# Performance work log

Hardware: AMD Instinct MI355X
Metric: run time of the kernel (lower is better)

Reference implementation:

```python
import jax, jax.numpy as jnp
import numpy as np

HIDDEN = 1024
HEADS = 16
HEAD_DIM = HIDDEN // HEADS


def setup_inputs() -> dict:
    key = jax.random.key(0)
    k1, k2, k3, k4, k5 = jax.random.split(key, 5)
    scale = 1.0 / np.sqrt(HIDDEN)
    return {
        "query": jax.random.normal(k1, (8, 1024, HIDDEN), dtype=jnp.float32),
        "w_qkv": jax.random.normal(k2, (HIDDEN, 3 * HIDDEN), dtype=jnp.float32) * scale,
        "b_qkv": jnp.zeros((3 * HIDDEN,), dtype=jnp.float32),
        "w_o": jax.random.normal(k3, (HIDDEN, HIDDEN), dtype=jnp.float32) * scale,
        "b_o": jnp.zeros((HIDDEN,), dtype=jnp.float32),
    }


def reference(query, w_qkv, b_qkv, w_o, b_o):
    B, S, _ = query.shape
    qkv = query @ w_qkv + b_qkv                      # [B,S,3H]
    q, k, v = jnp.split(qkv, 3, axis=-1)
    # split heads -> [B, heads, S, head_dim]
    def sh(x):
        return x.reshape(B, S, HEADS, HEAD_DIM).transpose(0, 2, 1, 3)
    qh, kh, vh = sh(q), sh(k), sh(v)
    qh = qh * (HEAD_DIM ** -0.5)
    logits = jnp.einsum("bhqd,bhkd->bhqk", qh, kh)   # [B,H,S,S]
    weights = jax.nn.softmax(logits, axis=-1)        # dropout p=0.0 -> identity
    x = jnp.einsum("bhqk,bhkd->bhqd", weights, vh)
    x = x.transpose(0, 2, 1, 3).reshape(B, S, HIDDEN)
    return x @ w_o + b_o
```

## Files before the change

kernel.cpp:

```cpp
#include <hip/hip_runtime.h>
#include <math.h>

#define BATCH   8
#define SEQ     1024
#define HIDDEN  1024
#define NHEADS  16
#define HDIM    64
#define MROWS   (BATCH * SEQ)

typedef __bf16 bf16x8 __attribute__((ext_vector_type(8)));
typedef float  f32x4  __attribute__((ext_vector_type(4)));

__device__ __forceinline__ unsigned short f2bf(float f) {
    union { float f; unsigned int u; } v; v.f = f;
    unsigned int u = v.u;
    u += 0x7fffu + ((u >> 16) & 1u);
    return (unsigned short)(u >> 16);
}

__device__ __forceinline__ unsigned int pack2bf_trunc(float a, float b) {
    union { float f; unsigned int u; } ua, ub;
    ua.f = a; ub.f = b;
    return (ua.u >> 16) | (ub.u & 0xFFFF0000u);
}

__device__ __forceinline__ void gl2lds16(const unsigned short* g, unsigned short* l) {
    __builtin_amdgcn_global_load_lds(
        (const __attribute__((address_space(1))) void*)g,
        (__attribute__((address_space(3))) void*)l, 16, 0, 0);
}

__global__ void cvt_f32_bf16_kernel(const float* __restrict__ in,
                                    unsigned short* __restrict__ out, int n4) {
    int i = blockIdx.x * blockDim.x + threadIdx.x;
    if (i < n4) {
        float4 v = reinterpret_cast<const float4*>(in)[i];
        ushort4 o;
        o.x = f2bf(v.x); o.y = f2bf(v.y); o.z = f2bf(v.z); o.w = f2bf(v.w);
        reinterpret_cast<ushort4*>(out)[i] = o;
    }
}

__global__ void transpose_cvt_kernel(const float* __restrict__ in,
                                     unsigned short* __restrict__ out,
                                     int R, int C) {
    __shared__ float tile[32][33];
    int x  = blockIdx.x * 32 + threadIdx.x;
    int y0 = blockIdx.y * 32;
#pragma unroll
    for (int j = 0; j < 32; j += 8)
        tile[threadIdx.y + j][threadIdx.x] = in[(size_t)(y0 + threadIdx.y + j) * C + x];
    __syncthreads();
    int x2 = y0 + threadIdx.x;
    int y2 = blockIdx.x * 32;
#pragma unroll
    for (int j = 0; j < 32; j += 8)
        out[(size_t)(y2 + threadIdx.y + j) * R + x2] = f2bf(tile[threadIdx.x][threadIdx.y + j]);
}

__global__ void transpose_v_kernel(const unsigned short* __restrict__ vin,
                                   unsigned short* __restrict__ vout) {
    __shared__ unsigned short tile[32][33];
    const int head = blockIdx.z;
    const int s0 = blockIdx.x * 32, d0 = blockIdx.y * 32;
    const unsigned short* src = vin + (size_t)head * SEQ * HDIM;
    unsigned short* dst = vout + (size_t)head * SEQ * HDIM;
    const int tx = threadIdx.x, ty = threadIdx.y;
#pragma unroll
    for (int j = 0; j < 32; j += 8)
        tile[ty + j][tx] = src[(size_t)(s0 + ty + j) * HDIM + d0 + tx];
    __syncthreads();
#pragma unroll
    for (int j = 0; j < 32; j += 8)
        dst[(size_t)(d0 + ty + j) * SEQ + s0 + tx] = tile[tx][ty + j];
}

template <int EPI>
__global__ __launch_bounds__(256) void gemm_bt_kernel(
    const unsigned short* __restrict__ A,
    const unsigned short* __restrict__ Bt,
    const float* __restrict__ bias,
    unsigned short* __restrict__ out_bf,
    float* __restrict__ out_f,
    int M, int N, int K) {
    __shared__ __align__(16) unsigned short As[128 * 64];
    __shared__ __align__(16) unsigned short Bs[128 * 64];

    const int tid  = threadIdx.x;
    const int wid  = tid >> 6;
    const int lane = tid & 63;
    const int l15  = lane & 15;
    const int quad = lane >> 4;
    const int wm   = (wid & 1) * 64;
    const int wn   = (wid >> 1) * 64;

    const int npn = N >> 7;
    const int pid = blockIdx.x;
    const int ppg = 4 * npn;
    const int gid = pid / ppg;
    const int loc = pid - gid * ppg;
    const int pm  = gid * 4 + (loc & 3);
    const int pn  = loc >> 2;
    const int m0  = pm * 128;
    const int n0  = pn * 128;

    const int srow = wid * 32 + (lane >> 3);
    const int skcs = ((lane & 7) ^ (lane >> 3)) * 8;
    const int rsw  = lane & 7;

    f32x4 acc[4][4];
#pragma unroll
    for (int i = 0; i < 4; ++i)
#pragma unroll
        for (int j = 0; j < 4; ++j) acc[i][j] = (f32x4){0.f, 0.f, 0.f, 0.f};

    for (int kt = 0; kt < K; kt += 64) {
        __syncthreads();
#pragma unroll
        for (int it = 0; it < 4; ++it) {
            int row = srow + it * 8;
            gl2lds16(A  + (size_t)(m0 + row) * K + kt + skcs, As + (wid * 32 + it * 8) * 64);
            gl2lds16(Bt + (size_t)(n0 + row) * K + kt + skcs, Bs + (wid * 32 + it * 8) * 64);
        }
        __syncthreads();
#pragma unroll
        for (int ks = 0; ks < 2; ++ks) {
            bf16x8 afr[4], bfr[4];
#pragma unroll
            for (int i = 0; i < 4; ++i)
                afr[i] = *reinterpret_cast<const bf16x8*>(
                    As + (wm + i * 16 + l15) * 64 + ((ks * 4 + quad) ^ rsw) * 8);
#pragma unroll
            for (int j = 0; j < 4; ++j)
                bfr[j] = *reinterpret_cast<const bf16x8*>(
                    Bs + (wn + j * 16 + l15) * 64 + ((ks * 4 + quad) ^ rsw) * 8);
#pragma unroll
            for (int i = 0; i < 4; ++i)
#pragma unroll
                for (int j = 0; j < 4; ++j)
                    acc[i][j] = __builtin_amdgcn_mfma_f32_16x16x32_bf16(afr[i], bfr[j], acc[i][j], 0, 0, 0);
        }
    }

#pragma unroll
    for (int j = 0; j < 4; ++j) {
        int col   = n0 + wn + j * 16 + l15;
        float bv  = bias[col];
        if constexpr (EPI == 0) {
            int which = col >> 10;
            int rem   = col & 1023;
            int h     = rem >> 6, d = rem & 63;
            float sc  = (which == 0) ? 0.18033688011112042f : 1.0f;
#pragma unroll
            for (int i = 0; i < 4; ++i)
#pragma unroll
                for (int r = 0; r < 4; ++r) {
                    int row = m0 + wm + i * 16 + quad * 4 + r;
                    int b   = row >> 10, s = row & 1023;
                    float v = (acc[i][j][r] + bv) * sc;
                    size_t idx = ((((size_t)which * BATCH + b) * NHEADS + h) * SEQ + s) * HDIM + d;
                    out_bf[idx] = f2bf(v);
                }
        } else {
#pragma unroll
            for (int i = 0; i < 4; ++i)
#pragma unroll
                for (int r = 0; r < 4; ++r) {
                    int row = m0 + wm + i * 16 + quad * 4 + r;
                    out_f[(size_t)row * N + col] = acc[i][j][r] + bv;
                }
        }
    }
}

__global__ __launch_bounds__(256, 4) void attn_kernel(
    const unsigned short* __restrict__ qkv,
    const unsigned short* __restrict__ vt,
    unsigned short* __restrict__ x) {
    constexpr int LDP = 68;
    __shared__ __align__(16) unsigned short Ks[64 * 64];
    __shared__ __align__(16) unsigned short Vs[64 * 64];
    __shared__ __align__(16) unsigned short PQ[4][32 * LDP];

    unsigned short* Qs = &PQ[0][0];

    const int tid  = threadIdx.x;
    const int wid  = tid >> 6;
    const int lane = tid & 63;
    const int l15  = lane & 15;
    const int quad = lane >> 4;
    const int srow8 = lane >> 3;
    const int skcs  = ((lane & 7) ^ srow8) * 8;
    const int rsw   = lane & 7;

    const int id = blockIdx.x;
    const int bh = (id & 7) * 16 + (id >> 6);
    const int q0 = ((id >> 3) & 7) * 128;

    const unsigned short* Qg  = qkv + (size_t)bh * SEQ * HDIM;
    const unsigned short* Kg  = qkv + (size_t)(128 + bh) * SEQ * HDIM;
    const unsigned short* VTg = vt + (size_t)bh * SEQ * HDIM;

#pragma unroll
    for (int it = 0; it < 4; ++it) {
        gl2lds16(Qg + (size_t)(q0 + wid * 32 + it * 8 + srow8) * HDIM + skcs,
                 Qs + (wid * 32 + it * 8) * 64);
    }
    __syncthreads();

    bf16x8 qf[2][2];
#pragma unroll
    for (int m = 0; m < 2; ++m)
#pragma unroll
        for (int h = 0; h < 2; ++h)
            qf[m][h] = *reinterpret_cast<const bf16x8*>(
                Qs + (wid * 32 + m * 16 + l15) * 64 + ((h * 4 + quad) ^ rsw) * 8);

    float lsum[2][4];
    f32x4 accO[2][4];
#pragma unroll
    for (int m = 0; m < 2; ++m)
#pragma unroll
        for (int r = 0; r < 4; ++r) lsum[m][r] = 0.f;
#pragma unroll
    for (int m = 0; m < 2; ++m)
#pragma unroll
        for (int jd = 0; jd < 4; ++jd) accO[m][jd] = (f32x4){0.f, 0.f, 0.f, 0.f};

    for (int t0 = 0; t0 < SEQ; t0 += 64) {
        __syncthreads();
#pragma unroll
        for (int it = 0; it < 2; ++it) {
            int row = wid * 16 + it * 8 + srow8;
            gl2lds16(Kg + (size_t)(t0 + row) * HDIM + skcs, Ks + (wid * 16 + it * 8) * 64);
            gl2lds16(VTg + (size_t)row * SEQ + t0 + skcs,   Vs + (wid * 16 + it * 8) * 64);
        }
        __syncthreads();

        f32x4 accL[2][4];
#pragma unroll
        for (int m = 0; m < 2; ++m)
#pragma unroll
            for (int j = 0; j < 4; ++j) accL[m][j] = (f32x4){0.f, 0.f, 0.f, 0.f};
#pragma unroll
        for (int j = 0; j < 4; ++j) {
            int krow = l15 * 4 + j;
            int kr7  = krow & 7;
            bf16x8 kf0 = *reinterpret_cast<const bf16x8*>(
                Ks + krow * 64 + ((0 + quad) ^ kr7) * 8);
            bf16x8 kf1 = *reinterpret_cast<const bf16x8*>(
                Ks + krow * 64 + ((4 + quad) ^ kr7) * 8);
#pragma unroll
            for (int m = 0; m < 2; ++m) {
                accL[m][j] = __builtin_amdgcn_mfma_f32_16x16x32_bf16(qf[m][0], kf0, accL[m][j], 0, 0, 0);
                accL[m][j] = __builtin_amdgcn_mfma_f32_16x16x32_bf16(qf[m][1], kf1, accL[m][j], 0, 0, 0);
            }
        }

#pragma unroll
        for (int m = 0; m < 2; ++m)
#pragma unroll
            for (int r = 0; r < 4; ++r) {
                float p0 = exp2f(accL[m][0][r]);
                float p1 = exp2f(accL[m][1][r]);
                float p2 = exp2f(accL[m][2][r]);
                float p3 = exp2f(accL[m][3][r]);
                lsum[m][r] += (p0 + p1) + (p2 + p3);
                uint2 pk;
                pk.x = pack2bf_trunc(p0, p1);
                pk.y = pack2bf_trunc(p2, p3);
                *reinterpret_cast<uint2*>(
                    &PQ[wid][(m * 16 + quad * 4 + r) * LDP + l15 * 4]) = pk;
            }

        bf16x8 pf[2][2];
#pragma unroll
        for (int m = 0; m < 2; ++m)
#pragma unroll
            for (int h = 0; h < 2; ++h)
                pf[m][h] = *reinterpret_cast<const bf16x8*>(
                    PQ[wid] + (m * 16 + l15) * LDP + h * 32 + quad * 8);
#pragma unroll
        for (int jd = 0; jd < 4; ++jd) {
            bf16x8 vf0 = *reinterpret_cast<const bf16x8*>(
                Vs + (jd * 16 + l15) * 64 + ((0 + quad) ^ rsw) * 8);
            bf16x8 vf1 = *reinterpret_cast<const bf16x8*>(
                Vs + (jd * 16 + l15) * 64 + ((4 + quad) ^ rsw) * 8);
#pragma unroll
            for (int m = 0; m < 2; ++m) {
                accO[m][jd] = __builtin_amdgcn_mfma_f32_16x16x32_bf16(pf[m][0], vf0, accO[m][jd], 0, 0, 0);
                accO[m][jd] = __builtin_amdgcn_mfma_f32_16x16x32_bf16(pf[m][1], vf1, accO[m][jd], 0, 0, 0);
            }
        }
    }

    const int b = bh >> 4, h = bh & 15;
#pragma unroll
    for (int m = 0; m < 2; ++m)
#pragma unroll
        for (int r = 0; r < 4; ++r) {
            float s = lsum[m][r];
            s += __shfl_xor(s, 1);
            s += __shfl_xor(s, 2);
            s += __shfl_xor(s, 4);
            s += __shfl_xor(s, 8);
            float inv = 1.0f / s;
            int srow = q0 + wid * 32 + m * 16 + quad * 4 + r;
            size_t base = ((size_t)b * SEQ + srow) * HIDDEN + h * HDIM;
#pragma unroll
            for (int jd = 0; jd < 4; ++jd)
                x[base + jd * 16 + l15] = f2bf(accO[m][jd][r] * inv);
        }
}

extern "C" void kernel_launch(void* const* d_in, const int* in_sizes, int n_in,
                              void* d_out, int out_size, void* d_ws, size_t ws_size,
                              hipStream_t stream) {
    const float* query = (const float*)d_in[0];
    const float* w_qkv = (const float*)d_in[1];
    const float* b_qkv = (const float*)d_in[2];
    const float* w_o   = (const float*)d_in[3];
    const float* b_o   = (const float*)d_in[4];
    float* out = (float*)d_out;

    unsigned short* ws = (unsigned short*)d_ws;
    unsigned short* queryBf = ws;
    unsigned short* wqkvT   = queryBf + (size_t)MROWS * HIDDEN;
    unsigned short* woT     = wqkvT + (size_t)3 * HIDDEN * HIDDEN;
    unsigned short* qkvbuf  = woT + (size_t)HIDDEN * HIDDEN;
    unsigned short* xbuf    = qkvbuf + (size_t)3 * MROWS * HIDDEN;
    unsigned short* vtbuf   = queryBf;

    cvt_f32_bf16_kernel<<<(MROWS * HIDDEN / 4 + 255) / 256, 256, 0, stream>>>(
        query, queryBf, MROWS * HIDDEN / 4);
    transpose_cvt_kernel<<<dim3(3 * HIDDEN / 32, HIDDEN / 32), dim3(32, 8), 0, stream>>>(
        w_qkv, wqkvT, HIDDEN, 3 * HIDDEN);
    transpose_cvt_kernel<<<dim3(HIDDEN / 32, HIDDEN / 32), dim3(32, 8), 0, stream>>>(
        w_o, woT, HIDDEN, HIDDEN);

    gemm_bt_kernel<0><<<dim3((MROWS / 128) * (3 * HIDDEN / 128)), 256, 0, stream>>>(
        queryBf, wqkvT, b_qkv, qkvbuf, nullptr, MROWS, 3 * HIDDEN, HIDDEN);

    transpose_v_kernel<<<dim3(SEQ / 32, HDIM / 32, BATCH * NHEADS), dim3(32, 8), 0, stream>>>(
        qkvbuf + (size_t)2 * BATCH * NHEADS * SEQ * HDIM, vtbuf);

    attn_kernel<<<dim3(1024), 256, 0, stream>>>(qkvbuf, vtbuf, xbuf);

    gemm_bt_kernel<1><<<dim3((MROWS / 128) * (HIDDEN / 128)), 256, 0, stream>>>(
        xbuf, woT, b_o, nullptr, out, MROWS, HIDDEN, HIDDEN);
}
```

Baseline: 255.4 us.

## Add 256x256-tile pipelined GEMM kernel for QKV projection

Adds a new GEMM kernel with 256x256 output tiles, 512 threads, a quad-buffered LDS staging scheme with direct global-to-LDS loads, XOR swizzle, and interleaved MFMA phases with priority hints. It also maps blocks to XCDs so each XCD works on a contiguous band of M tiles. It is used only for the QKV projection and is meant to raise data reuse and overlap loads with MFMA work. The trade-off is heavier register and LDS use, which limits occupancy, and the grid has fewer blocks (384).

```diff
diff --git a/kernel.cpp b/kernel.cpp
--- a/kernel.cpp
+++ b/kernel.cpp
@@ -169,6 +169,196 @@
                     int row = m0 + wm + i * 16 + quad * 4 + r;
                     out_f[(size_t)row * N + col] = acc[i][j][r] + bv;
                 }
+        }
+    }
+}
+
+template <int EPI>
+__global__ __launch_bounds__(512, 2) void gemm256_kernel(
+    const unsigned short* __restrict__ A,
+    const unsigned short* __restrict__ Bt,
+    const float* __restrict__ bias,
+    unsigned short* __restrict__ out_bf,
+    float* __restrict__ out_f,
+    int M, int N, int K) {
+    __shared__ __align__(16) unsigned short As[4 * 128 * 64];
+    __shared__ __align__(16) unsigned short Bs[4 * 128 * 64];
+
+    const int tid  = threadIdx.x;
+    const int wid  = tid >> 6;
+    const int lane = tid & 63;
+    const int l15  = lane & 15;
+    const int quad = lane >> 4;
+    const int wm   = wid & 1;
+    const int wn   = wid >> 1;
+    const int rsw  = lane & 7;
+
+    const int npm = M >> 8;
+    const int bpx = npm >> 3;
+    const int id  = blockIdx.x;
+    const int xcd = id & 7;
+    const int loc = id >> 3;
+    const int pm  = xcd * bpx + (loc % bpx);
+    const int pn  = loc / bpx;
+    const int m0  = pm << 8;
+    const int n0  = pn << 8;
+
+    const int    srow = wid * 8 + (lane >> 3);
+    const int    skc  = ((lane & 7) ^ (lane >> 3)) * 8;
+    const size_t K64r = (size_t)64 * K;
+    const unsigned short* aT = A  + (size_t)(m0 + srow) * K + skc;
+    const unsigned short* bT = Bt + (size_t)(n0 + srow) * K + skc;
+
+    auto stA = [&](int tt, int half) {
+        unsigned short* d = As + (((tt << 1) + half) & 3) * 8192 + wid * 512;
+        const unsigned short* s = aT + (size_t)(half * 2) * K64r + tt * 64;
+        gl2lds16(s, d);
+        gl2lds16(s + K64r, d + 4096);
+    };
+    auto stB = [&](int tt, int half) {
+        unsigned short* d = Bs + (((tt << 1) + half) & 3) * 8192 + wid * 512;
+        const unsigned short* s = bT + (size_t)(half * 2) * K64r + tt * 64;
+        gl2lds16(s, d);
+        gl2lds16(s + K64r, d + 4096);
+    };
+
+    auto ldA4 = [&](int p, int half, bf16x8 (&a)[4][2]) {
+        const unsigned short* s = As + (p * 2 + half) * 8192 + (wm * 64 + l15) * 64;
+#pragma unroll
+        for (int i = 0; i < 4; ++i)
+#pragma unroll
+            for (int ks = 0; ks < 2; ++ks)
+                a[i][ks] = *reinterpret_cast<const bf16x8*>(
+                    s + i * 16 * 64 + ((ks * 4 + quad) ^ rsw) * 8);
+    };
+    auto ldB2 = [&](int p, int half, bf16x8 (&b)[2][2]) {
+        const unsigned short* s = Bs + (p * 2 + half) * 8192 + (wn * 32 + l15) * 64;
+#pragma unroll
+        for (int j = 0; j < 2; ++j)
+#pragma unroll
+            for (int ks = 0; ks < 2; ++ks)
+                b[j][ks] = *reinterpret_cast<const bf16x8*>(
+                    s + j * 16 * 64 + ((ks * 4 + quad) ^ rsw) * 8);
+    };
+
+    f32x4 acc[8][4];
+#pragma unroll
+    for (int i = 0; i < 8; ++i)
+#pragma unroll
+        for (int j = 0; j < 4; ++j) acc[i][j] = (f32x4){0.f, 0.f, 0.f, 0.f};
+
+    const int NT = K >> 6;
+
+    stA(0, 0); stA(0, 1); stB(0, 0); stB(0, 1);
+    stA(1, 0); stB(1, 0); stB(1, 1);
+    asm volatile("s_waitcnt vmcnt(6)" ::: "memory");
+    __builtin_amdgcn_s_barrier();
+    asm volatile("" ::: "memory");
+
+    bf16x8 a[4][2], b0[2][2], b1[2][2];
+
+    for (int t = 0; t < NT; ++t) {
+        const int p = t & 1;
+
+        ldA4(p, 0, a);
+        ldB2(p, 0, b0);
+        if (t + 1 < NT) stA(t + 1, 1);
+        __builtin_amdgcn_s_barrier();
+        asm volatile("s_waitcnt lgkmcnt(0)" ::: "memory");
+        __builtin_amdgcn_s_setprio(1);
+#pragma unroll
+        for (int ks = 0; ks < 2; ++ks)
+#pragma unroll
+            for (int i = 0; i < 4; ++i)
+#pragma unroll
+                for (int j = 0; j < 2; ++j)
+                    acc[i][j] = __builtin_amdgcn_mfma_f32_16x16x32_bf16(
+                        a[i][ks], b0[j][ks], acc[i][j], 0, 0, 0);
+        __builtin_amdgcn_s_setprio(0);
+        __builtin_amdgcn_s_barrier();
+        asm volatile("" ::: "memory");
+
+        ldB2(p, 1, b1);
+        if (t + 2 < NT) stA(t + 2, 0);
+        __builtin_amdgcn_s_barrier();
+        asm volatile("s_waitcnt lgkmcnt(0)" ::: "memory");
+        __builtin_amdgcn_s_setprio(1);
+#pragma unroll
+        for (int ks = 0; ks < 2; ++ks)
+#pragma unroll
+            for (int i = 0; i < 4; ++i)
+#pragma unroll
+                for (int j = 0; j < 2; ++j)
+                    acc[i][2 + j] = __builtin_amdgcn_mfma_f32_16x16x32_bf16(
+                        a[i][ks], b1[j][ks], acc[i][2 + j], 0, 0, 0);
+        __builtin_amdgcn_s_setprio(0);
+        __builtin_amdgcn_s_barrier();
+        asm volatile("" ::: "memory");
+
+        ldA4(p, 1, a);
+        if (t + 2 < NT) stB(t + 2, 0);
+        __builtin_amdgcn_s_barrier();
+        asm volatile("s_waitcnt lgkmcnt(0)" ::: "memory");
+        __builtin_amdgcn_s_setprio(1);
+#pragma unroll
+        for (int ks = 0; ks < 2; ++ks)
+#pragma unroll
+            for (int i = 0; i < 4; ++i)
+#pragma unroll
+                for (int j = 0; j < 2; ++j)
+                    acc[4 + i][j] = __builtin_amdgcn_mfma_f32_16x16x32_bf16(
+                        a[i][ks], b0[j][ks], acc[4 + i][j], 0, 0, 0);
+        __builtin_amdgcn_s_setprio(0);
+        __builtin_amdgcn_s_barrier();
+        asm volatile("" ::: "memory");
+
+        if (t + 2 < NT) {
+            stB(t + 2, 1);
+            asm volatile("s_waitcnt vmcnt(6)" ::: "memory");
+        } else {
+            asm volatile("s_waitcnt vmcnt(0)" ::: "memory");
+        }
+        __builtin_amdgcn_s_barrier();
+        asm volatile("" ::: "memory");
+        __builtin_amdgcn_s_setprio(1);
+#pragma unroll
+        for (int ks = 0; ks < 2; ++ks)
+#pragma unroll
+            for (int i = 0; i < 4; ++i)
+#pragma unroll
+                for (int j = 0; j < 2; ++j)
+                    acc[4 + i][2 + j] = __builtin_amdgcn_mfma_f32_16x16x32_bf16(
+                        a[i][ks], b1[j][ks], acc[4 + i][2 + j], 0, 0, 0);
+        __builtin_amdgcn_s_setprio(0);
+        __builtin_amdgcn_s_barrier();
+        asm volatile("" ::: "memory");
+    }
+
+#pragma unroll
+    for (int mi = 0; mi < 8; ++mi) {
+        const int rowb = m0 + (mi & 4) * 32 + wm * 64 + (mi & 3) * 16 + quad * 4;
+#pragma unroll
+        for (int nj = 0; nj < 4; ++nj) {
+            const int col = n0 + (nj & 2) * 64 + wn * 32 + (nj & 1) * 16 + l15;
+            const float bv = bias[col];
+            if constexpr (EPI == 0) {
+                const int which = col >> 10;
+                const int h = (col & 1023) >> 6, d = col & 63;
+                const float sc = (which == 0) ? 0.18033688011112042f : 1.0f;
+#pragma unroll
+                for (int r = 0; r < 4; ++r) {
+                    const int row = rowb + r;
+                    const int b = row >> 10, s = row & 1023;
+                    const float v = (acc[mi][nj][r] + bv) * sc;
+                    const size_t idx =
+                        ((((size_t)which * BATCH + b) * NHEADS + h) * SEQ + s) * HDIM + d;
+                    out_bf[idx] = f2bf(v);
+                }
+            } else {
+#pragma unroll
+                for (int r = 0; r < 4; ++r)
+                    out_f[(size_t)(rowb + r) * N + col] = acc[mi][nj][r] + bv;
+            }
         }
     }
 }
@@ -338,7 +528,7 @@
     transpose_cvt_kernel<<<dim3(HIDDEN / 32, HIDDEN / 32), dim3(32, 8), 0, stream>>>(
         w_o, woT, HIDDEN, HIDDEN);
 
-    gemm_bt_kernel<0><<<dim3((MROWS / 128) * (3 * HIDDEN / 128)), 256, 0, stream>>>(
+    gemm256_kernel<0><<<dim3((MROWS / 256) * (3 * HIDDEN / 256)), 512, 0, stream>>>(
         queryBf, wqkvT, b_qkv, qkvbuf, nullptr, MROWS, 3 * HIDDEN, HIDDEN);
 
     transpose_v_kernel<<<dim3(SEQ / 32, HDIM / 32, BATCH * NHEADS), dim3(32, 8), 0, stream>>>(
```

Result: no change. 258.1 us (+1.1%).

## Fuse prep conversions into one kernel and write V transposed from QKV GEMM

Applied to the files above, without the earlier changes.

Merges the query cast and both weight transpose-casts into a single prep launch, which removes two kernel launches. The QKV GEMM epilogue now writes the V slice directly in [head, d, seq] layout using 8-byte ushort4 stores, so the separate V transpose kernel and its extra read/write pass over V are gone. The cost is longer-strided stores in the V epilogue.

```diff
diff --git a/kernel.cpp b/kernel.cpp
--- a/kernel.cpp
+++ b/kernel.cpp
@@ -30,49 +30,47 @@
         (__attribute__((address_space(3))) void*)l, 16, 0, 0);
 }
 
-__global__ void cvt_f32_bf16_kernel(const float* __restrict__ in,
-                                    unsigned short* __restrict__ out, int n4) {
-    int i = blockIdx.x * blockDim.x + threadIdx.x;
-    if (i < n4) {
-        float4 v = reinterpret_cast<const float4*>(in)[i];
+__global__ __launch_bounds__(256) void prep_kernel(
+    const float* __restrict__ query, unsigned short* __restrict__ queryBf,
+    const float* __restrict__ wqkv,  unsigned short* __restrict__ wqkvT,
+    const float* __restrict__ wo,    unsigned short* __restrict__ woT) {
+    __shared__ float tile[32][33];
+    const int bid = blockIdx.x;
+    const int tid = threadIdx.x;
+
+    if (bid < 8192) {
+        int i = bid * 256 + tid;
+        float4 v = reinterpret_cast<const float4*>(query)[i];
         ushort4 o;
         o.x = f2bf(v.x); o.y = f2bf(v.y); o.z = f2bf(v.z); o.w = f2bf(v.w);
-        reinterpret_cast<ushort4*>(out)[i] = o;
-    }
-}
-
-__global__ void transpose_cvt_kernel(const float* __restrict__ in,
-                                     unsigned short* __restrict__ out,
-                                     int R, int C) {
-    __shared__ float tile[32][33];
-    int x  = blockIdx.x * 32 + threadIdx.x;
-    int y0 = blockIdx.y * 32;
+        reinterpret_cast<ushort4*>(queryBf)[i] = o;
+        return;
+    }
+
+    const float* in;
+    unsigned short* out;
+    int R, C, bx, by;
+    if (bid < 8192 + 3072) {
+        int b = bid - 8192;
+        in = wqkv; out = wqkvT; R = HIDDEN; C = 3 * HIDDEN;
+        bx = b % 96; by = b / 96;
+    } else {
+        int b = bid - 11264;
+        in = wo; out = woT; R = HIDDEN; C = HIDDEN;
+        bx = b % 32; by = b / 32;
+    }
+    const int tx = tid & 31, ty = tid >> 5;
+    const int x  = bx * 32 + tx;
+    const int y0 = by * 32;
 #pragma unroll
     for (int j = 0; j < 32; j += 8)
-        tile[threadIdx.y + j][threadIdx.x] = in[(size_t)(y0 + threadIdx.y + j) * C + x];
+        tile[ty + j][tx] = in[(size_t)(y0 + ty + j) * C + x];
     __syncthreads();
-    int x2 = y0 + threadIdx.x;
-    int y2 = blockIdx.x * 32;
+    const int x2 = y0 + tx;
+    const int y2 = bx * 32;
 #pragma unroll
     for (int j = 0; j < 32; j += 8)
-        out[(size_t)(y2 + threadIdx.y + j) * R + x2] = f2bf(tile[threadIdx.x][threadIdx.y + j]);
-}
-
-__global__ void transpose_v_kernel(const unsigned short* __restrict__ vin,
-                                   unsigned short* __restrict__ vout) {
-    __shared__ unsigned short tile[32][33];
-    const int head = blockIdx.z;
-    const int s0 = blockIdx.x * 32, d0 = blockIdx.y * 32;
-    const unsigned short* src = vin + (size_t)head * SEQ * HDIM;
-    unsigned short* dst = vout + (size_t)head * SEQ * HDIM;
-    const int tx = threadIdx.x, ty = threadIdx.y;
-#pragma unroll
-    for (int j = 0; j < 32; j += 8)
-        tile[ty + j][tx] = src[(size_t)(s0 + ty + j) * HDIM + d0 + tx];
-    __syncthreads();
-#pragma unroll
-    for (int j = 0; j < 32; j += 8)
-        dst[(size_t)(d0 + ty + j) * SEQ + s0 + tx] = tile[tx][ty + j];
+        out[(size_t)(y2 + ty + j) * R + x2] = f2bf(tile[tx][ty + j]);
 }
 
 template <int EPI>
@@ -150,17 +148,34 @@
             int which = col >> 10;
             int rem   = col & 1023;
             int h     = rem >> 6, d = rem & 63;
-            float sc  = (which == 0) ? 0.18033688011112042f : 1.0f;
-#pragma unroll
-            for (int i = 0; i < 4; ++i)
-#pragma unroll
-                for (int r = 0; r < 4; ++r) {
-                    int row = m0 + wm + i * 16 + quad * 4 + r;
-                    int b   = row >> 10, s = row & 1023;
-                    float v = (acc[i][j][r] + bv) * sc;
-                    size_t idx = ((((size_t)which * BATCH + b) * NHEADS + h) * SEQ + s) * HDIM + d;
-                    out_bf[idx] = f2bf(v);
+            if (which == 2) {
+#pragma unroll
+                for (int i = 0; i < 4; ++i) {
+                    int row0 = m0 + wm + i * 16 + quad * 4;
+                    int b    = row0 >> 10, s0 = row0 & 1023;
+                    ushort4 o;
+                    o.x = f2bf(acc[i][j][0] + bv);
+                    o.y = f2bf(acc[i][j][1] + bv);
+                    o.z = f2bf(acc[i][j][2] + bv);
+                    o.w = f2bf(acc[i][j][3] + bv);
+                    size_t idx = ((size_t)(2 * BATCH * NHEADS) +
+                                  (size_t)b * NHEADS + h) * (SEQ * HDIM) +
+                                 (size_t)d * SEQ + s0;
+                    *reinterpret_cast<ushort4*>(out_bf + idx) = o;
                 }
+            } else {
+                float sc = (which == 0) ? 0.18033688011112042f : 1.0f;
+#pragma unroll
+                for (int i = 0; i < 4; ++i)
+#pragma unroll
+                    for (int r = 0; r < 4; ++r) {
+                        int row = m0 + wm + i * 16 + quad * 4 + r;
+                        int b   = row >> 10, s = row & 1023;
+                        float v = (acc[i][j][r] + bv) * sc;
+                        size_t idx = ((((size_t)which * BATCH + b) * NHEADS + h) * SEQ + s) * HDIM + d;
+                        out_bf[idx] = f2bf(v);
+                    }
+            }
         } else {
 #pragma unroll
             for (int i = 0; i < 4; ++i)
@@ -329,21 +344,14 @@
     unsigned short* woT     = wqkvT + (size_t)3 * HIDDEN * HIDDEN;
     unsigned short* qkvbuf  = woT + (size_t)HIDDEN * HIDDEN;
     unsigned short* xbuf    = qkvbuf + (size_t)3 * MROWS * HIDDEN;
-    unsigned short* vtbuf   = queryBf;
-
-    cvt_f32_bf16_kernel<<<(MROWS * HIDDEN / 4 + 255) / 256, 256, 0, stream>>>(
-        query, queryBf, MROWS * HIDDEN / 4);
-    transpose_cvt_kernel<<<dim3(3 * HIDDEN / 32, HIDDEN / 32), dim3(32, 8), 0, stream>>>(
-        w_qkv, wqkvT, HIDDEN, 3 * HIDDEN);
-    transpose_cvt_kernel<<<dim3(HIDDEN / 32, HIDDEN / 32), dim3(32, 8), 0, stream>>>(
-        w_o, woT, HIDDEN, HIDDEN);
+    unsigned short* vtbuf   = qkvbuf + (size_t)2 * BATCH * NHEADS * SEQ * HDIM;
+
+    prep_kernel<<<dim3(12288), 256, 0, stream>>>(
+        query, queryBf, w_qkv, wqkvT, w_o, woT);
 
     gemm_bt_kernel<0><<<dim3((MROWS / 128) * (3 * HIDDEN / 128)), 256, 0, stream>>>(
         queryBf, wqkvT, b_qkv, qkvbuf, nullptr, MROWS, 3 * HIDDEN, HIDDEN);
 
-    transpose_v_kernel<<<dim3(SEQ / 32, HDIM / 32, BATCH * NHEADS), dim3(32, 8), 0, stream>>>(
-        qkvbuf + (size_t)2 * BATCH * NHEADS * SEQ * HDIM, vtbuf);
-
     attn_kernel<<<dim3(1024), 256, 0, stream>>>(qkvbuf, vtbuf, xbuf);
 
     gemm_bt_kernel<1><<<dim3((MROWS / 128) * (HIDDEN / 128)), 256, 0, stream>>>(
```

Measured after the change: 237.4 us. 7.1% less time.
